# Performance work log

Hardware: AMD Instinct MI355X
Metric: run time of the kernel (lower is better)

The kernel has to match this reference:

```python
import jax, jax.numpy as jnp
import numpy as np

S = 64       # n_subdomains
N = 131072   # n_points
D = 2        # in_dim (t, x)
H = 32       # hidden
SCALE, SHIFT = 1.0, 0.0  # unnorm_para


def setup_inputs() -> dict:
    key = jax.random.key(0)
    ks = jax.random.split(key, 10)
    # --- subdomain geometry: tile x in [-1,1] into S overlapping cells, t spans [0,1]
    edges = np.linspace(-1.0, 1.0, S + 1)
    cell = edges[1] - edges[0]
    lo_core = np.stack([np.zeros(S), edges[:-1]], axis=1)   # (S,2) = [t_lo, x_lo]
    hi_core = np.stack([np.ones(S), edges[1:]], axis=1)
    lo_ext = lo_core - np.array([0.1, 0.3 * cell])
    hi_ext = hi_core + np.array([0.1, 0.3 * cell])
    # --- collocation points: t ~ U[0,1], x ~ U[-1,1]
    u01 = jax.random.uniform(ks[0], (N, D), dtype=jnp.float32)
    x = u01 * jnp.array([1.0, 2.0], jnp.float32) + jnp.array([0.0, -1.0], jnp.float32)
    # --- stacked per-subdomain MLP params (in->H, H->H, H->H, H->1), tanh activations
    def init(k, shape, fan_in):
        return (jax.random.normal(k, shape, dtype=jnp.float32) / np.sqrt(fan_in)).astype(jnp.float32)
    return {
        "x": x,
        "lo_core": jnp.asarray(lo_core, jnp.float32),
        "hi_core": jnp.asarray(hi_core, jnp.float32),
        "lo_ext": jnp.asarray(lo_ext, jnp.float32),
        "hi_ext": jnp.asarray(hi_ext, jnp.float32),
        "W_in": init(ks[1], (S, H, D), D),
        "b_in": jnp.zeros((S, H), jnp.float32),
        "W_h1": init(ks[2], (S, H, H), H),
        "b_h1": jnp.zeros((S, H), jnp.float32),
        "W_h2": init(ks[3], (S, H, H), H),
        "b_h2": jnp.zeros((S, H), jnp.float32),
        "W_out": init(ks[4], (S, 1, H), H),
        "b_out": jnp.zeros((S, 1), jnp.float32),
    }


def reference(x, lo_core, hi_core, lo_ext, hi_ext,
              W_in, b_in, W_h1, b_h1, W_h2, b_h2, W_out, b_out):
    # 1) per-subdomain normalization of x to [-1,1]:  (S,N,D)
    center = (lo_ext + hi_ext) * 0.5
    half_w = (hi_ext - lo_ext) * 0.5
    xn = (x[None, :, :] - center[:, None, :]) / half_w[:, None, :]
    # 2) all tiny subnet MLPs evaluated in one batched pass (vmap equivalent)
    h = jnp.tanh(jnp.einsum('snd,shd->snh', xn, W_in) + b_in[:, None, :])
    h = jnp.tanh(jnp.einsum('snh,skh->snk', h, W_h1) + b_h1[:, None, :])
    h = jnp.tanh(jnp.einsum('snh,skh->snk', h, W_h2) + b_h2[:, None, :])
    out = jnp.einsum('snh,soh->sno', h, W_out) + b_out[:, None, :]   # (S,N,1)
    out = out * SCALE + SHIFT  # unnorm
    # 3) sigmoid-product window per subdomain: (S,N,1)
    overlap = jnp.maximum(hi_ext - hi_core, lo_core - lo_ext)       # (S,D)
    width = hi_ext - lo_ext
    s = 4.0 / (2.0 * overlap * width + 1e-8)                        # (S,D)
    left = jax.nn.sigmoid(s[:, None, :] * (x[None, :, :] - lo_core[:, None, :]))
    right = jax.nn.sigmoid(s[:, None, :] * (hi_core[:, None, :] - x[None, :, :]))
    w = jnp.prod(left * right, axis=-1, keepdims=True)              # (S,N,1)
    w = w / (jnp.sum(w, axis=0, keepdims=True) + 1e-8)
    # 4) weighted sum across subdomains
    u = jnp.sum(out * w, axis=0)                                    # (N,1)
    # 5) hard BC constraint: -sin(pi*x) + tanh(x+1)tanh(x-1)tanh(t)*u
    g = -jnp.sin(jnp.pi * x[:, 1])[:, None]
    factor = (jnp.tanh(x[:, 1] + 1.0) * jnp.tanh(x[:, 1] - 1.0) * jnp.tanh(x[:, 0]))[:, None]
    return g + factor * u
```

## Files before the change

kernel.cpp:

```cpp
#include <hip/hip_runtime.h>
#include <math.h>

namespace {
constexpr int S = 64;
constexpr int NP = 131072;
constexpr int H = 32;
constexpr int BLK = 256;
constexpr int NBK = 3 * S;
constexpr int NBH = 64;
constexpr int PPB = NP / NBH;
constexpr int NCH_MAX = 6400;

typedef float v2f __attribute__((ext_vector_type(2)));

constexpr int WS_OFF  = 0;
constexpr int WS_NCH  = 193;
constexpr int WS_BH   = 194;
constexpr int WS_LIST = WS_BH + NBH * NBK;
constexpr int WS_XS   = WS_LIST + NP;
constexpr int WS_PART = WS_XS + 2 * NP;
constexpr int WS_DESC = WS_PART + 6 * NP;

__device__ __forceinline__ float dev_exp2(float v) {
    return __builtin_amdgcn_exp2f(v);
}
__device__ __forceinline__ float fast_tanh(float v) {
    float e = dev_exp2(v * 2.8853900817779268f);
    return 1.0f - __fdividef(2.0f, e + 1.0f);
}
__device__ __forceinline__ float fast_sigmoid(float z) {
    return __fdividef(1.0f, 1.0f + dev_exp2(z * -1.4426950408889634f));
}
__device__ __forceinline__ void cell_band(float xx, int& c, float& frac) {
    float pos = (xx + 1.0f) * 32.0f;
    c = min(S - 1, max(0, (int)floorf(pos)));
    frac = pos - (float)c;
}
__device__ __forceinline__ int band_of(float frac) {
    return (frac > 0.33f ? 1 : 0) + (frac > 0.67f ? 1 : 0);
}

__global__ __launch_bounds__(BLK) void k_hist(const float2* __restrict__ x,
                                              int* __restrict__ blockhist) {
    __shared__ int lh[NBK];
    const int tid = threadIdx.x;
    if (tid < NBK) lh[tid] = 0;
    __syncthreads();
    const int pbase = blockIdx.x * PPB;
    for (int t = tid; t < PPB; t += BLK) {
        int c; float frac;
        cell_band(x[pbase + t].y, c, frac);
        atomicAdd(&lh[3 * c + band_of(frac)], 1);
    }
    __syncthreads();
    if (tid < NBK) blockhist[blockIdx.x * NBK + tid] = lh[tid];
}

__global__ __launch_bounds__(NBK) void k_scan(int* __restrict__ blockhist,
                                              int* __restrict__ off,
                                              int* __restrict__ nch,
                                              int2* __restrict__ desc) {
    __shared__ int loff[NBK + 1];
    __shared__ int wsum[3];
    __shared__ int wsum2[3];
    const int t = threadIdx.x;
    int tot = 0;
    for (int b = 0; b < NBH; ++b) tot += blockhist[b * NBK + t];
    int incl = tot;
    #pragma unroll
    for (int d = 1; d < 64; d <<= 1) {
        int o = __shfl_up(incl, d);
        if ((t & 63) >= d) incl += o;
    }
    if ((t & 63) == 63) wsum[t >> 6] = incl;
    __syncthreads();
    int pre = 0;
    for (int w = 0; w < (t >> 6); ++w) pre += wsum[w];
    const int o = pre + incl - tot;
    off[t] = o;  loff[t] = o;
    if (t == NBK - 1) { off[NBK] = pre + incl; loff[NBK] = pre + incl; }
    int run = o;
    for (int b = 0; b < NBH; ++b) {
        int v = blockhist[b * NBK + t];
        blockhist[b * NBK + t] = run;
        run += v;
    }
    __syncthreads();

    const int j = t / 3;
    const int z = t - 3 * j;
    int lo2 = 0, hi2 = 0;
    if (z == 0)                { lo2 = loff[3*j];   hi2 = loff[3*j+3]; }
    else if (z == 1 && j+1 < S){ lo2 = loff[3*j+3]; hi2 = loff[3*j+5]; }
    else if (z == 2 && j > 0)  { lo2 = loff[3*j-2]; hi2 = loff[3*j]; }
    const int cnt = hi2 - lo2;
    const int cc  = (cnt + 63) >> 6;
    int incl2 = cc;
    #pragma unroll
    for (int d = 1; d < 64; d <<= 1) {
        int o2 = __shfl_up(incl2, d);
        if ((t & 63) >= d) incl2 += o2;
    }
    if ((t & 63) == 63) wsum2[t >> 6] = incl2;
    __syncthreads();
    int pre2 = 0;
    for (int w = 0; w < (t >> 6); ++w) pre2 += wsum2[w];
    const int pos = pre2 + incl2 - cc;
    if (t == NBK - 1) nch[0] = pre2 + incl2;
    for (int i = 0; i < cc; ++i) {
        const int rem = cnt - (i << 6);
        const int len = rem < 64 ? rem : 64;
        desc[pos + i] = make_int2(lo2 + (i << 6), len | (j << 8) | (z << 16));
    }
}

__global__ __launch_bounds__(BLK) void k_scatter(const float* __restrict__ x,
                                                 const int* __restrict__ base,
                                                 int* __restrict__ list,
                                                 float2* __restrict__ xsorted) {
    __shared__ int lh[NBK];
    __shared__ int lbase[NBK];
    const int tid = threadIdx.x;
    if (tid < NBK) { lh[tid] = 0; lbase[tid] = base[blockIdx.x * NBK + tid]; }
    __syncthreads();
    const int pbase = blockIdx.x * PPB;
    for (int t = tid; t < PPB; t += BLK) {
        const int p = pbase + t;
        const float2 xv = ((const float2*)x)[p];
        int c; float frac;
        cell_band(xv.y, c, frac);
        const int k = 3 * c + band_of(frac);
        const int r = atomicAdd(&lh[k], 1);
        const int pos = lbase[k] + r;
        list[pos] = p;
        xsorted[pos] = xv;
    }
}

__global__ __launch_bounds__(64, 4) void k_main(
    const float2* __restrict__ xsorted,
    const float* __restrict__ lo_core, const float* __restrict__ hi_core,
    const float* __restrict__ lo_ext,  const float* __restrict__ hi_ext,
    const float* __restrict__ W_in,  const float* __restrict__ b_in,
    const float* __restrict__ W_h1,  const float* __restrict__ b_h1,
    const float* __restrict__ W_h2,  const float* __restrict__ b_h2,
    const float* __restrict__ W_out, const float* __restrict__ b_out,
    const int* __restrict__ nch, const int2* __restrict__ desc,
    float2* __restrict__ part)
{
    const int lane = threadIdx.x;
    const int w = blockIdx.x;
    if (w >= nch[0]) return;
    const int2 d = desc[w];
    const int slot0 = __builtin_amdgcn_readfirstlane(d.x);
    const int meta  = __builtin_amdgcn_readfirstlane(d.y);
    const int len = meta & 255;
    const int j   = (meta >> 8) & 255;
    const int z   = meta >> 16;
    const bool act = lane < len;
    const int slot = slot0 + (act ? lane : len - 1);
    const float2 xv = xsorted[slot];
    const float tt = xv.x, xx = xv.y;

    const float le0 = lo_ext[2*j+0], he0 = hi_ext[2*j+0];
    const float le1 = lo_ext[2*j+1], he1 = hi_ext[2*j+1];
    const float ic0 = (le0 + he0) * 0.5f, ih0 = __fdividef(1.0f, (he0 - le0) * 0.5f);
    const float ic1 = (le1 + he1) * 0.5f, ih1 = __fdividef(1.0f, (he1 - le1) * 0.5f);
    const v2f xn = {(tt - ic0) * ih0, (xx - ic1) * ih1};

    v2f h0[H/2], h1[H/2];

    {
        const v2f* Wiv = (const v2f*)(W_in + j * (H * 2));
        const float* bi = b_in + j * H;
        #pragma unroll
        for (int k2 = 0; k2 < H/2; ++k2) {
            v2f aA = __builtin_elementwise_fma(xn, Wiv[2*k2+0], (v2f){bi[2*k2+0], 0.0f});
            v2f aB = __builtin_elementwise_fma(xn, Wiv[2*k2+1], (v2f){bi[2*k2+1], 0.0f});
            h0[k2] = (v2f){fast_tanh(aA.x + aA.y), fast_tanh(aB.x + aB.y)};
        }
    }
    {
        const v2f* W1v = (const v2f*)(W_h1 + j * (H * H));
        const float* b1 = b_h1 + j * H;
        #pragma unroll
        for (int k2 = 0; k2 < H/2; ++k2) {
            const v2f* rowA = W1v + (2*k2) * (H/2);
            const v2f* rowB = rowA + (H/2);
            v2f aA = {b1[2*k2+0], 0.0f};
            v2f aB = {b1[2*k2+1], 0.0f};
            #pragma unroll
            for (int q2 = 0; q2 < H/2; ++q2) {
                aA = __builtin_elementwise_fma(h0[q2], rowA[q2], aA);
                aB = __builtin_elementwise_fma(h0[q2], rowB[q2], aB);
            }
            h1[k2] = (v2f){fast_tanh(aA.x + aA.y), fast_tanh(aB.x + aB.y)};
        }
    }
    {
        const v2f* W2v = (const v2f*)(W_h2 + j * (H * H));
        const float* b2 = b_h2 + j * H;
        #pragma unroll
        for (int k2 = 0; k2 < H/2; ++k2) {
            const v2f* rowA = W2v + (2*k2) * (H/2);
            const v2f* rowB = rowA + (H/2);
            v2f aA = {b2[2*k2+0], 0.0f};
            v2f aB = {b2[2*k2+1], 0.0f};
            #pragma unroll
            for (int q2 = 0; q2 < H/2; ++q2) {
                aA = __builtin_elementwise_fma(h1[q2], rowA[q2], aA);
                aB = __builtin_elementwise_fma(h1[q2], rowB[q2], aB);
            }
            h0[k2] = (v2f){fast_tanh(aA.x + aA.y), fast_tanh(aB.x + aB.y)};
        }
    }
    float acc;
    {
        const v2f* Wov = (const v2f*)(W_out + j * H);
        v2f a = {b_out[j], 0.0f};
        #pragma unroll
        for (int q2 = 0; q2 < H/2; ++q2) {
            a = __builtin_elementwise_fma(h0[q2], Wov[q2], a);
        }
        acc = a.x + a.y;
    }

    float w2 = 1.0f;
    {
        const float lc = lo_core[2*j+0], hc = hi_core[2*j+0];
        const float ov = fmaxf(he0 - hc, lc - le0);
        const float sc = __fdividef(4.0f, fmaf(2.0f * ov, he0 - le0, 1e-8f));
        w2 *= fast_sigmoid(sc * (tt - lc)) * fast_sigmoid(sc * (hc - tt));
    }
    {
        const float lc = lo_core[2*j+1], hc = hi_core[2*j+1];
        const float ov = fmaxf(he1 - hc, lc - le1);
        const float sc = __fdividef(4.0f, fmaf(2.0f * ov, he1 - le1, 1e-8f));
        w2 *= fast_sigmoid(sc * (xx - lc)) * fast_sigmoid(sc * (hc - xx));
    }
    if (act) part[z * NP + slot] = make_float2(acc * w2, w2);
}

__global__ __launch_bounds__(BLK) void k_combine(
    const float2* __restrict__ part,
    const float2* __restrict__ xsorted,
    const int* __restrict__ list,
    float* __restrict__ out)
{
    const int i = blockIdx.x * BLK + threadIdx.x;
    const float2 xv = xsorted[i];
    const float tt = xv.x, xx = xv.y;
    int c; float frac;
    cell_band(xx, c, frac);
    float nsum = 0.0f, dsum = 0.0f;
    if (c > 0 && !(frac > 0.67f)) {
        const float2 p1 = part[NP + i];
        nsum = p1.x; dsum = p1.y;
    }
    const float2 p0 = part[i];
    nsum += p0.x; dsum += p0.y;
    if (c < S - 1 && frac > 0.33f) {
        const float2 p2 = part[2 * NP + i];
        nsum += p2.x; dsum += p2.y;
    }
    const float u = __fdividef(nsum, dsum + 1e-8f);
    const float g = -sinf(3.14159265358979323846f * xx);
    const float factor = fast_tanh(xx + 1.0f) * fast_tanh(xx - 1.0f) * fast_tanh(tt);
    out[list[i]] = fmaf(factor, u, g);
}
}

extern "C" void kernel_launch(void* const* d_in, const int* in_sizes, int n_in,
                              void* d_out, int out_size, void* d_ws, size_t ws_size,
                              hipStream_t stream) {
    const float* x       = (const float*)d_in[0];
    const float* lo_core = (const float*)d_in[1];
    const float* hi_core = (const float*)d_in[2];
    const float* lo_ext  = (const float*)d_in[3];
    const float* hi_ext  = (const float*)d_in[4];
    const float* W_in    = (const float*)d_in[5];
    const float* b_in    = (const float*)d_in[6];
    const float* W_h1    = (const float*)d_in[7];
    const float* b_h1    = (const float*)d_in[8];
    const float* W_h2    = (const float*)d_in[9];
    const float* b_h2    = (const float*)d_in[10];
    const float* W_out   = (const float*)d_in[11];
    const float* b_out   = (const float*)d_in[12];
    float* out = (float*)d_out;

    int* ws        = (int*)d_ws;
    int* off       = ws + WS_OFF;
    int* nch       = ws + WS_NCH;
    int* blockhist = ws + WS_BH;
    int* list      = ws + WS_LIST;
    float2* xsorted = (float2*)(ws + WS_XS);
    float2* part    = (float2*)(ws + WS_PART);
    int2*   desc    = (int2*)(ws + WS_DESC);

    hipLaunchKernelGGL(k_hist,    dim3(NBH),      dim3(BLK), 0, stream, (const float2*)x, blockhist);
    hipLaunchKernelGGL(k_scan,    dim3(1),        dim3(NBK), 0, stream, blockhist, off, nch, desc);
    hipLaunchKernelGGL(k_scatter, dim3(NBH),      dim3(BLK), 0, stream, x, blockhist, list, xsorted);
    hipLaunchKernelGGL(k_main,    dim3(NCH_MAX),  dim3(64),  0, stream,
        xsorted, lo_core, hi_core, lo_ext, hi_ext, W_in, b_in, W_h1, b_h1,
        W_h2, b_h2, W_out, b_out, nch, desc, part);
    hipLaunchKernelGGL(k_combine, dim3(NP / BLK), dim3(BLK), 0, stream, part, xsorted, list, out);
}
```

Before: 57.41 us.

## Replace per-block histogram scan with global atomic histogram and cursor reservation

The counting-sort preprocessing now accumulates a single global histogram with atomics instead of storing per-block histograms that the single-block scan kernel had to read serially over 64 blocks. The scatter kernel reserves its output ranges by atomically bumping a global cursor per bucket, so the scan no longer computes per-block bases. The point loops are also unrolled and kept in registers. This removes the serial 64-iteration loops in the one-block scan, but adds a memset launch and makes the order within each bucket nondeterministic.

```diff
diff --git a/kernel.cpp b/kernel.cpp
--- a/kernel.cpp
+++ b/kernel.cpp
@@ -9,14 +9,16 @@
 constexpr int NBK = 3 * S;
 constexpr int NBH = 64;
 constexpr int PPB = NP / NBH;
+constexpr int PPT = PPB / BLK;
 constexpr int NCH_MAX = 6400;
 
 typedef float v2f __attribute__((ext_vector_type(2)));
 
 constexpr int WS_OFF  = 0;
 constexpr int WS_NCH  = 193;
-constexpr int WS_BH   = 194;
-constexpr int WS_LIST = WS_BH + NBH * NBK;
+constexpr int WS_HIST = 194;
+constexpr int WS_CUR  = 386;
+constexpr int WS_LIST = 578;
 constexpr int WS_XS   = WS_LIST + NP;
 constexpr int WS_PART = WS_XS + 2 * NP;
 constexpr int WS_DESC = WS_PART + 6 * NP;
@@ -41,31 +43,32 @@
 }
 
 __global__ __launch_bounds__(BLK) void k_hist(const float2* __restrict__ x,
-                                              int* __restrict__ blockhist) {
+                                              int* __restrict__ hist) {
     __shared__ int lh[NBK];
     const int tid = threadIdx.x;
     if (tid < NBK) lh[tid] = 0;
     __syncthreads();
     const int pbase = blockIdx.x * PPB;
-    for (int t = tid; t < PPB; t += BLK) {
+    #pragma unroll
+    for (int i = 0; i < PPT; ++i) {
         int c; float frac;
-        cell_band(x[pbase + t].y, c, frac);
+        cell_band(x[pbase + i * BLK + tid].y, c, frac);
         atomicAdd(&lh[3 * c + band_of(frac)], 1);
     }
     __syncthreads();
-    if (tid < NBK) blockhist[blockIdx.x * NBK + tid] = lh[tid];
-}
-
-__global__ __launch_bounds__(NBK) void k_scan(int* __restrict__ blockhist,
+    if (tid < NBK && lh[tid] != 0) atomicAdd(&hist[tid], lh[tid]);
+}
+
+__global__ __launch_bounds__(NBK) void k_scan(const int* __restrict__ hist,
                                               int* __restrict__ off,
+                                              int* __restrict__ cursor,
                                               int* __restrict__ nch,
                                               int2* __restrict__ desc) {
     __shared__ int loff[NBK + 1];
     __shared__ int wsum[3];
     __shared__ int wsum2[3];
     const int t = threadIdx.x;
-    int tot = 0;
-    for (int b = 0; b < NBH; ++b) tot += blockhist[b * NBK + t];
+    const int tot = hist[t];
     int incl = tot;
     #pragma unroll
     for (int d = 1; d < 64; d <<= 1) {
@@ -77,14 +80,8 @@
     int pre = 0;
     for (int w = 0; w < (t >> 6); ++w) pre += wsum[w];
     const int o = pre + incl - tot;
-    off[t] = o;  loff[t] = o;
+    off[t] = o;  cursor[t] = o;  loff[t] = o;
     if (t == NBK - 1) { off[NBK] = pre + incl; loff[NBK] = pre + incl; }
-    int run = o;
-    for (int b = 0; b < NBH; ++b) {
-        int v = blockhist[b * NBK + t];
-        blockhist[b * NBK + t] = run;
-        run += v;
-    }
     __syncthreads();
 
     const int j = t / 3;
@@ -114,26 +111,35 @@
     }
 }
 
-__global__ __launch_bounds__(BLK) void k_scatter(const float* __restrict__ x,
-                                                 const int* __restrict__ base,
+__global__ __launch_bounds__(BLK) void k_scatter(const float2* __restrict__ x,
+                                                 int* __restrict__ cursor,
                                                  int* __restrict__ list,
                                                  float2* __restrict__ xsorted) {
     __shared__ int lh[NBK];
     __shared__ int lbase[NBK];
     const int tid = threadIdx.x;
-    if (tid < NBK) { lh[tid] = 0; lbase[tid] = base[blockIdx.x * NBK + tid]; }
+    if (tid < NBK) lh[tid] = 0;
     __syncthreads();
     const int pbase = blockIdx.x * PPB;
-    for (int t = tid; t < PPB; t += BLK) {
-        const int p = pbase + t;
-        const float2 xv = ((const float2*)x)[p];
+    float2 xv[PPT];
+    int    kk[PPT];
+    int    rr[PPT];
+    #pragma unroll
+    for (int i = 0; i < PPT; ++i) {
+        xv[i] = x[pbase + i * BLK + tid];
         int c; float frac;
-        cell_band(xv.y, c, frac);
-        const int k = 3 * c + band_of(frac);
-        const int r = atomicAdd(&lh[k], 1);
-        const int pos = lbase[k] + r;
-        list[pos] = p;
-        xsorted[pos] = xv;
+        cell_band(xv[i].y, c, frac);
+        kk[i] = 3 * c + band_of(frac);
+        rr[i] = atomicAdd(&lh[kk[i]], 1);
+    }
+    __syncthreads();
+    if (tid < NBK && lh[tid] != 0) lbase[tid] = atomicAdd(&cursor[tid], lh[tid]);
+    __syncthreads();
+    #pragma unroll
+    for (int i = 0; i < PPT; ++i) {
+        const int pos = lbase[kk[i]] + rr[i];
+        list[pos] = pbase + i * BLK + tid;
+        xsorted[pos] = xv[i];
     }
 }
 
@@ -288,18 +294,20 @@
     const float* b_out   = (const float*)d_in[12];
     float* out = (float*)d_out;
 
-    int* ws        = (int*)d_ws;
-    int* off       = ws + WS_OFF;
-    int* nch       = ws + WS_NCH;
-    int* blockhist = ws + WS_BH;
-    int* list      = ws + WS_LIST;
+    int* ws      = (int*)d_ws;
+    int* off     = ws + WS_OFF;
+    int* nch     = ws + WS_NCH;
+    int* hist    = ws + WS_HIST;
+    int* cursor  = ws + WS_CUR;
+    int* list    = ws + WS_LIST;
     float2* xsorted = (float2*)(ws + WS_XS);
     float2* part    = (float2*)(ws + WS_PART);
     int2*   desc    = (int2*)(ws + WS_DESC);
 
-    hipLaunchKernelGGL(k_hist,    dim3(NBH),      dim3(BLK), 0, stream, (const float2*)x, blockhist);
-    hipLaunchKernelGGL(k_scan,    dim3(1),        dim3(NBK), 0, stream, blockhist, off, nch, desc);
-    hipLaunchKernelGGL(k_scatter, dim3(NBH),      dim3(BLK), 0, stream, x, blockhist, list, xsorted);
+    hipMemsetAsync(hist, 0, NBK * sizeof(int), stream);
+    hipLaunchKernelGGL(k_hist,    dim3(NBH),      dim3(BLK), 0, stream, (const float2*)x, hist);
+    hipLaunchKernelGGL(k_scan,    dim3(1),        dim3(NBK), 0, stream, hist, off, cursor, nch, desc);
+    hipLaunchKernelGGL(k_scatter, dim3(NBH),      dim3(BLK), 0, stream, (const float2*)x, cursor, list, xsorted);
     hipLaunchKernelGGL(k_main,    dim3(NCH_MAX),  dim3(64),  0, stream,
         xsorted, lo_core, hi_core, lo_ext, hi_ext, W_in, b_in, W_h1, b_h1,
         W_h2, b_h2, W_out, b_out, nch, desc, part);
```

Result: slower. 64.68 us (+12.7%).
